# Optimization experiments

Measured on AMD Instinct MI355X. Metric: run time of the kernel, lower is better.

Reference implementation:

```python
import jax, jax.numpy as jnp
import numpy as np

D = 512  # link/path state dim == GRU hidden
R = 256  # readout dim
T = 8    # message-passing steps


def gru_cell(x, h, W_ih, W_hh, b_ih, b_hh):
    # torch nn.GRU cell math (weights stored [3H, in])
    gi = x @ W_ih.T + b_ih
    gh = h @ W_hh.T + b_hh
    i_r, i_z, i_n = jnp.split(gi, 3, axis=-1)
    h_r, h_z, h_n = jnp.split(gh, 3, axis=-1)
    r = jax.nn.sigmoid(i_r + h_r)
    z = jax.nn.sigmoid(i_z + h_z)
    n = jnp.tanh(i_n + r * h_n)
    return (1.0 - z) * n + z * h


def setup_inputs():
    key = jax.random.key(0)
    n_links, n_paths, L = 2000, 20000, 6
    ks = jax.random.split(key, 24)
    links = jax.random.randint(ks[0], (n_paths * L,), 0, n_links)
    paths = jnp.repeat(jnp.arange(n_paths), L)   # path id per entry
    seqs = jnp.tile(jnp.arange(L), n_paths)      # position of link within path
    link_capacity = jax.random.uniform(ks[1], (n_links, 1))
    bandwidth = jax.random.uniform(ks[2], (n_paths, 1))

    def u(k, shape, fan_in):
        s = 1.0 / np.sqrt(fan_in)
        return jax.random.uniform(k, shape, minval=-s, maxval=s)

    inp = dict(links=links, paths=paths, seqs=seqs,
               link_capacity=link_capacity, bandwidth=bandwidth)
    # path GRU (p_U) and link GRU (l_U)
    inp['Wih_p'] = u(ks[3], (3 * D, D), D); inp['Whh_p'] = u(ks[4], (3 * D, D), D)
    inp['bih_p'] = u(ks[5], (3 * D,), D);   inp['bhh_p'] = u(ks[6], (3 * D,), D)
    inp['Wih_l'] = u(ks[7], (3 * D, D), D); inp['Whh_l'] = u(ks[8], (3 * D, D), D)
    inp['bih_l'] = u(ks[9], (3 * D,), D);   inp['bhh_l'] = u(ks[10], (3 * D,), D)
    # readout MLPs (delay + jitter), torch Linear layout [out, in]
    inp['d_w1'] = u(ks[11], (R, D), D);      inp['d_b1'] = u(ks[12], (R,), D)
    inp['d_w2'] = u(ks[13], (R // 2, R), R); inp['d_b2'] = u(ks[14], (R // 2,), R)
    inp['d_w3'] = u(ks[15], (1, R // 2), R // 2); inp['d_b3'] = u(ks[16], (1,), R // 2)
    inp['j_w1'] = u(ks[17], (R, D), D);      inp['j_b1'] = u(ks[18], (R,), D)
    inp['j_w2'] = u(ks[19], (R // 2, R), R); inp['j_b2'] = u(ks[20], (R // 2,), R)
    inp['j_w3'] = u(ks[21], (1, R // 2), R // 2); inp['j_b3'] = u(ks[22], (1,), R // 2)
    inp['n_links'] = n_links
    inp['n_paths'] = n_paths
    inp['max_seq_len'] = L  # == max(seqs)+1
    return inp


def mlp(x, w1, b1, w2, b2, w3, b3):
    h = jax.nn.relu(x @ w1.T + b1)
    h = jax.nn.relu(h @ w2.T + b2)
    return h @ w3.T + b3


def reference(links, paths, seqs, link_capacity, bandwidth,
              Wih_p, Whh_p, bih_p, bhh_p, Wih_l, Whh_l, bih_l, bhh_l,
              d_w1, d_b1, d_w2, d_b2, d_w3, d_b3,
              j_w1, j_b1, j_w2, j_b2, j_w3, j_b3,
              n_links, n_paths, max_seq_len):
    dt = bandwidth.dtype
    path_h = jnp.concatenate([bandwidth, jnp.zeros((n_paths, D - 1), dt)], axis=1)
    link_h = jnp.concatenate([link_capacity, jnp.zeros((n_links, D - 1), dt)], axis=1)

    def p_step(h, x_t):
        h2 = gru_cell(x_t, h, Wih_p, Whh_p, bih_p, bhh_p)
        return h2, h2

    for _ in range(T):
        h_lp = link_h[links]  # gather link states onto path entries [E, D]
        x_seq = jnp.zeros((n_paths, max_seq_len, D), dt).at[paths, seqs].set(h_lp)
        path_h, outs = jax.lax.scan(p_step, path_h, jnp.swapaxes(x_seq, 0, 1))
        outs = jnp.swapaxes(outs, 0, 1)  # [n_paths, L, D] per-step path states
        msg = outs[paths, seqs]          # [E, D] message from each path position
        agg = jax.ops.segment_sum(msg, links, num_segments=n_links)  # scatter-add
        link_h = gru_cell(agg, link_h, Wih_l, Whh_l, bih_l, bhh_l)

    d = mlp(path_h, d_w1, d_b1, d_w2, d_b2, d_w3, d_b3)
    j = mlp(path_h, j_w1, j_b1, j_w2, j_b2, j_w3, j_b3)
    return d, j
```

## Files before the change

kernel.cpp:

```cpp
#include <hip/hip_runtime.h>
#include <stdint.h>

typedef __attribute__((ext_vector_type(4))) float float4v;
typedef __attribute__((ext_vector_type(2))) float float2v;
typedef __attribute__((ext_vector_type(8))) short short8v;

static __device__ __forceinline__ float sigp(float x){ return 1.f/(1.f+expf(-x)); }

static __device__ __forceinline__ unsigned short f2bf(float x){
  unsigned u = __float_as_uint(x);
  u += 0x7FFFu + ((u>>16)&1u);
  return (unsigned short)(u>>16);
}
static __device__ __forceinline__ float bf2f(unsigned short h){
  return __uint_as_float(((unsigned)h)<<16);
}

static __device__ __forceinline__ void gload16(const void* g, void* l){
  __builtin_amdgcn_global_load_lds((const __attribute__((address_space(1))) void*)g,
                                   (__attribute__((address_space(3))) void*)l, 16, 0, 0);
}

__global__ void sentf_k(float* __restrict__ o, int n, float v){
  int i = blockIdx.x*256 + threadIdx.x; if (i < n) o[i] = v;
}

__global__ void prep_k(const int* __restrict__ links, const int* __restrict__ paths,
                       const int* __restrict__ seqs, int* __restrict__ plink,
                       int* __restrict__ cnt){
  int e = blockIdx.x*256 + threadIdx.x;
  if (e < 120000){
    int p = paths[e], s = seqs[e], l = links[e];
    plink[p*6 + s] = l;
    atomicAdd(&cnt[s*2000 + l], 1);
  }
}
__global__ void scan_k(const int* __restrict__ cnt, int* __restrict__ off, int* __restrict__ cur){
  __shared__ int part[256]; __shared__ int pref[256];
  int t = threadIdx.x;
  int lo = t*47, hi = lo+47; if (hi > 12000) hi = 12000;
  int s = 0;
  for (int i=lo;i<hi;i++) s += cnt[i];
  part[t] = s; __syncthreads();
  if (t==0){ int r=0; for (int i=0;i<256;i++){ pref[i]=r; r+=part[i]; } }
  __syncthreads();
  int r = pref[t];
  for (int i=lo;i<hi;i++){ off[i]=r; cur[i]=r; r+=cnt[i]; }
}
__global__ void fill2_k(const int* __restrict__ links, const int* __restrict__ paths,
                        const int* __restrict__ seqs, int* __restrict__ cur,
                        int* __restrict__ plist){
  int e = blockIdx.x*256 + threadIdx.x;
  if (e < 120000){
    int p = paths[e], s = seqs[e], l = links[e];
    int pos = atomicAdd(&cur[s*2000 + l], 1);
    plist[pos] = p;
  }
}

__global__ void wcvt_k(const float* __restrict__ W, unsigned short* __restrict__ hi,
                       unsigned short* __restrict__ lo, int n){
  int i = blockIdx.x*256 + threadIdx.x;
  if (i < n){
    float x = W[i];
    unsigned short h = f2bf(x);
    hi[i] = h;
    lo[i] = f2bf(x - bf2f(h));
  }
}

__global__ void initp_k(const float* __restrict__ x0,
                        unsigned short* __restrict__ h0, unsigned short* __restrict__ l0,
                        unsigned short* __restrict__ h1, unsigned short* __restrict__ l1,
                        int Mreal){
  int i = blockIdx.x*256 + threadIdx.x;
  int m = i >> 9, c = i & 511;
  float v = (c==0 && m < Mreal) ? x0[m] : 0.f;
  unsigned short hh = f2bf(v);
  unsigned short ll = f2bf(v - bf2f(hh));
  h0[i]=hh; l0[i]=ll; h1[i]=hh; l1[i]=ll;
}

__global__ __launch_bounds__(512,4) void gmfma_k(
    const unsigned short* __restrict__ Ahi, const unsigned short* __restrict__ Alo,
    const unsigned short* __restrict__ Whi, const unsigned short* __restrict__ Wlo,
    const float* __restrict__ bias, const float* __restrict__ GI,
    const int* __restrict__ plink, int s,
    float* __restrict__ OutF,
    unsigned short* __restrict__ Ohi, unsigned short* __restrict__ Olo,
    int M, int gru, int writeF)
{
  __shared__ unsigned short sAh0[128*32], sAl0[128*32];
  __shared__ unsigned short sBh0[192*32], sBl0[192*32];
  __shared__ unsigned short sAh1[128*32], sAl1[128*32];
  __shared__ unsigned short sBh1[192*32], sBl1[192*32];
  const int tid  = threadIdx.x;
  const int lane = tid & 63, wave = tid >> 6;
  const int wm = wave >> 2, wn = wave & 3;
  const int bid = blockIdx.x;
  const int X = bid & 7, kk2 = bid >> 3;
  const int m0 = ((kk2 >> 3)*8 + X) * 128;
  const int cb = kk2 & 7;
  const int c16 = lane & 15, kq = lane >> 4;

  int offA;
  {
    int row = tid >> 2; int kg = (tid & 3) ^ ((row >> 1) & 3);
    offA = (m0 + row)*1024 + kg*16;
  }
  int offB0, offB1;
  {
    int gb = tid;
    int v  = gb >> 2;
    int kg = (gb & 3) ^ ((v >> 1) & 3);
    int wn_ = v / 48; int rem = v - wn_*48;
    int gg = rem >> 4, cc = rem & 15;
    offB0 = (gg*512 + cb*64 + wn_*16 + cc)*1024 + kg*16;
    gb = 512 + tid;
    v  = gb >> 2;
    kg = (gb & 3) ^ ((v >> 1) & 3);
    int wn2 = v / 48; rem = v - wn2*48;
    gg = rem >> 4; cc = rem & 15;
    if (wn2 > 3) wn2 = 3;
    offB1 = (gg*512 + cb*64 + wn2*16 + cc)*1024 + kg*16;
  }
  const int gA  = (wave*64)*8;
  const int gB0 = (wave*64)*8, gB1 = (512 + wave*64)*8;

  const int rA = wm*64 + c16;
  const int rdA = (rA*4 + (kq ^ ((rA>>1)&3)))*8;
  const int vB = wn*48 + c16;
  const int rdB = (vB*4 + (kq ^ ((vB>>1)&3)))*8;

  float4v acc[4][3];
#pragma unroll
  for (int i = 0; i < 4; ++i)
#pragma unroll
    for (int j = 0; j < 3; ++j) acc[i][j] = (float4v){0.f,0.f,0.f,0.f};

  auto STAGE = [&](int kb, unsigned short* dAh, unsigned short* dAl,
                   unsigned short* dBh, unsigned short* dBl){
    const int kbb = kb*64;
    const char* ah = (const char*)Ahi + kbb;
    const char* al = (const char*)Alo + kbb;
    const char* wh = (const char*)Whi + kbb;
    const char* wl = (const char*)Wlo + kbb;
    gload16(ah + offA, dAh + gA);
    gload16(al + offA, dAl + gA);
    gload16(wh + offB0, dBh + gB0);
    gload16(wl + offB0, dBl + gB0);
    if (tid < 256){
      gload16(wh + offB1, dBh + gB1);
      gload16(wl + offB1, dBl + gB1);
    }
  };

  auto COMPUTE = [&](const unsigned short* tAh, const unsigned short* tAl,
                     const unsigned short* tBh, const unsigned short* tBl){
    short8v ah[4], al[4], bh[3], bl[3];
#pragma unroll
    for (int mf = 0; mf < 4; ++mf) ah[mf] = *(const short8v*)(tAh + rdA + mf*512);
#pragma unroll
    for (int g = 0; g < 3; ++g)  bh[g]  = *(const short8v*)(tBh + rdB + g*512);
#pragma unroll
    for (int mf = 0; mf < 4; ++mf) al[mf] = *(const short8v*)(tAl + rdA + mf*512);
#pragma unroll
    for (int mf = 0; mf < 4; ++mf)
#pragma unroll
      for (int g = 0; g < 3; ++g)
        acc[mf][g] = __builtin_amdgcn_mfma_f32_16x16x32_bf16(ah[mf], bh[g], acc[mf][g], 0, 0, 0);
#pragma unroll
    for (int g = 0; g < 3; ++g)  bl[g]  = *(const short8v*)(tBl + rdB + g*512);
#pragma unroll
    for (int mf = 0; mf < 4; ++mf)
#pragma unroll
      for (int g = 0; g < 3; ++g)
        acc[mf][g] = __builtin_amdgcn_mfma_f32_16x16x32_bf16(al[mf], bh[g], acc[mf][g], 0, 0, 0);
#pragma unroll
    for (int mf = 0; mf < 4; ++mf)
#pragma unroll
      for (int g = 0; g < 3; ++g)
        acc[mf][g] = __builtin_amdgcn_mfma_f32_16x16x32_bf16(ah[mf], bl[g], acc[mf][g], 0, 0, 0);
  };

  STAGE(0, sAh0, sAl0, sBh0, sBl0);
  __syncthreads();
  for (int q = 0; q < 8; ++q){
    STAGE(2*q+1, sAh1, sAl1, sBh1, sBl1);
    COMPUTE(sAh0, sAl0, sBh0, sBl0);
    __syncthreads();
    if (q < 7) STAGE(2*q+2, sAh0, sAl0, sBh0, sBl0);
    COMPUTE(sAh1, sAl1, sBh1, sBl1);
    __syncthreads();
  }

  const int col = cb*64 + wn*16 + c16;
  if (!gru){
    const float b0f = bias[col], b1f = bias[512+col], b2f = bias[1024+col];
#pragma unroll
    for (int mf = 0; mf < 4; ++mf){
      const int mb = m0 + wm*64 + mf*16 + kq*4;
#pragma unroll
      for (int r = 0; r < 4; ++r){
        const int m = mb + r;
        if (m < M){
          float* c = OutF + (size_t)m*1536 + col;
          c[0]    = acc[mf][0][r] + b0f;
          c[512]  = acc[mf][1][r] + b1f;
          c[1024] = acc[mf][2][r] + b2f;
        }
      }
    }
  } else {
    const float br = bias[col], bz = bias[512+col], bn = bias[1024+col];
#pragma unroll
    for (int mf = 0; mf < 4; ++mf){
      const int mb = m0 + wm*64 + mf*16 + kq*4;
#pragma unroll
      for (int r = 0; r < 4; ++r){
        const int m = mb + r;
        if (m < M){
          const int gr = plink ? plink[m*6 + s] : m;
          const float* gi = GI + (size_t)gr*1536 + col;
          const size_t ix = (size_t)m*512 + col;
          float hold = bf2f(Ahi[ix]) + bf2f(Alo[ix]);
          float rr = sigp(gi[0]    + acc[mf][0][r] + br);
          float zz = sigp(gi[512]  + acc[mf][1][r] + bz);
          float nn = 2.f*sigp(2.f*(gi[1024] + rr*(acc[mf][2][r] + bn))) - 1.f;
          float h  = (1.f - zz)*nn + zz*hold;
          unsigned short hh = f2bf(h);
          Ohi[ix] = hh;
          Olo[ix] = f2bf(h - bf2f(hh));
          if (writeF) OutF[ix] = h;
        }
      }
    }
  }
}

__global__ __launch_bounds__(256,3) void rgemm_k(
    const unsigned short* __restrict__ Ahi, const unsigned short* __restrict__ Alo,
    const unsigned short* __restrict__ Whi, const unsigned short* __restrict__ Wlo,
    const float* __restrict__ bias,
    float* __restrict__ OutF,
    unsigned short* __restrict__ Ohi, unsigned short* __restrict__ Olo,
    int M, int N, int K, int relu)
{
  __shared__ unsigned short rAh0[128*32], rAl0[128*32], rWh0[64*32], rWl0[64*32];
  __shared__ unsigned short rAh1[128*32], rAl1[128*32], rWh1[64*32], rWl1[64*32];
  const int tid = threadIdx.x;
  const int lane = tid & 63, wave = tid >> 6;
  const int wm = wave >> 1, wn = wave & 1;
  const int m0 = blockIdx.x * 128, n0 = blockIdx.y * 64;
  const int c16 = lane & 15, kq = lane >> 4;
  const int K2 = K*2;

  int offA0, offA1, offW;
  { int g = tid;      int row = g>>2; int kg=(g&3)^((row>>1)&3); offA0 = (m0+row)*K2 + kg*16; }
  { int g = tid+256;  int row = g>>2; int kg=(g&3)^((row>>1)&3); offA1 = (m0+row)*K2 + kg*16; }
  { int g = tid;      int v = g>>2;   int kg=(g&3)^((v>>1)&3);   offW  = (n0+v)*K2 + kg*16; }
  const int gA0 = (wave*64)*8, gA1 = (wave*64+256)*8;
  const int gW  = (wave*64)*8;

  const int rA = wm*64 + c16;
  const int rdA = (rA*4 + (kq ^ ((rA>>1)&3)))*8;
  const int vB = wn*32 + c16;
  const int rdB = (vB*4 + (kq ^ ((vB>>1)&3)))*8;

  float4v acc[4][2];
#pragma unroll
  for (int i = 0; i < 4; ++i)
#pragma unroll
    for (int j = 0; j < 2; ++j) acc[i][j] = (float4v){0.f,0.f,0.f,0.f};

  auto STAGE = [&](int kb, unsigned short* dAh, unsigned short* dAl,
                   unsigned short* dWh, unsigned short* dWl){
    const int kbb = kb*64;
    gload16((const char*)Ahi + kbb + offA0, dAh + gA0);
    gload16((const char*)Ahi + kbb + offA1, dAh + gA1);
    gload16((const char*)Alo + kbb + offA0, dAl + gA0);
    gload16((const char*)Alo + kbb + offA1, dAl + gA1);
    gload16((const char*)Whi + kbb + offW, dWh + gW);
    gload16((const char*)Wlo + kbb + offW, dWl + gW);
  };

  auto COMPUTE = [&](const unsigned short* tAh, const unsigned short* tAl,
                     const unsigned short* tWh, const unsigned short* tWl){
    short8v ah[4], al[4], bh[2], bl[2];
#pragma unroll
    for (int mf = 0; mf < 4; ++mf) ah[mf] = *(const short8v*)(tAh + rdA + mf*512);
#pragma unroll
    for (int nf = 0; nf < 2; ++nf) bh[nf] = *(const short8v*)(tWh + rdB + nf*512);
#pragma unroll
    for (int mf = 0; mf < 4; ++mf) al[mf] = *(const short8v*)(tAl + rdA + mf*512);
#pragma unroll
    for (int mf = 0; mf < 4; ++mf)
#pragma unroll
      for (int nf = 0; nf < 2; ++nf)
        acc[mf][nf] = __builtin_amdgcn_mfma_f32_16x16x32_bf16(ah[mf], bh[nf], acc[mf][nf], 0, 0, 0);
#pragma unroll
    for (int nf = 0; nf < 2; ++nf) bl[nf] = *(const short8v*)(tWl + rdB + nf*512);
#pragma unroll
    for (int mf = 0; mf < 4; ++mf)
#pragma unroll
      for (int nf = 0; nf < 2; ++nf)
        acc[mf][nf] = __builtin_amdgcn_mfma_f32_16x16x32_bf16(al[mf], bh[nf], acc[mf][nf], 0, 0, 0);
#pragma unroll
    for (int mf = 0; mf < 4; ++mf)
#pragma unroll
      for (int nf = 0; nf < 2; ++nf)
        acc[mf][nf] = __builtin_amdgcn_mfma_f32_16x16x32_bf16(ah[mf], bl[nf], acc[mf][nf], 0, 0, 0);
  };

  const int nc = K >> 5;
  STAGE(0, rAh0, rAl0, rWh0, rWl0);
  __syncthreads();
  for (int q = 0; q < (nc>>1); ++q){
    STAGE(2*q+1, rAh1, rAl1, rWh1, rWl1);
    COMPUTE(rAh0, rAl0, rWh0, rWl0);
    __syncthreads();
    if (q < (nc>>1)-1) STAGE(2*q+2, rAh0, rAl0, rWh0, rWl0);
    COMPUTE(rAh1, rAl1, rWh1, rWl1);
    __syncthreads();
  }

#pragma unroll
  for (int nf = 0; nf < 2; ++nf){
    const int col = n0 + wn*32 + nf*16 + c16;
    const float b = bias[col];
#pragma unroll
    for (int mf = 0; mf < 4; ++mf){
      const int mb = m0 + wm*64 + mf*16 + kq*4;
#pragma unroll
      for (int r = 0; r < 4; ++r){
        const int m = mb + r;
        if (m < M){
          float v = acc[mf][nf][r] + b;
          if (relu) v = fmaxf(v, 0.f);
          const size_t ix = (size_t)m*N + col;
          if (OutF) OutF[ix] = v;
          if (Ohi){
            unsigned short hh = f2bf(v);
            Ohi[ix] = hh;
            Olo[ix] = f2bf(v - bf2f(hh));
          }
        }
      }
    }
  }
}

__global__ void aggv_k(const unsigned short* __restrict__ Hh, const unsigned short* __restrict__ Hl,
                       const int* __restrict__ plist,
                       const int* __restrict__ off, const int* __restrict__ cnt, int s,
                       float* __restrict__ AGG, int isFirst,
                       unsigned short* __restrict__ Ghi, unsigned short* __restrict__ Glo,
                       int emit)
{
  int l = blockIdx.x, t = threadIdx.x;
  size_t base = (size_t)l*512 + 2*t;
  if (l >= 2000){
    AGG[base] = 0.f; AGG[base+1] = 0.f;
    if (emit){ *(unsigned*)&Ghi[base] = 0u; *(unsigned*)&Glo[base] = 0u; }
    return;
  }
  int o = off[s*2000 + l], c = cnt[s*2000 + l];
  float a0 = isFirst ? 0.f : AGG[base];
  float a1 = isFirst ? 0.f : AGG[base+1];
  for (int i = 0; i < c; ++i){
    size_t p = (size_t)plist[o + i] * 512 + 2*t;
    unsigned hh = *(const unsigned*)(Hh + p);
    unsigned hl = *(const unsigned*)(Hl + p);
    a0 += __uint_as_float(hh << 16) + __uint_as_float(hl << 16);
    a1 += __uint_as_float(hh & 0xffff0000u) + __uint_as_float(hl & 0xffff0000u);
  }
  AGG[base] = a0; AGG[base+1] = a1;
  if (emit){
    unsigned short h0 = f2bf(a0), h1 = f2bf(a1);
    *(unsigned*)&Ghi[base] = (unsigned)h0 | ((unsigned)h1 << 16);
    unsigned short l0 = f2bf(a0 - bf2f(h0)), l1 = f2bf(a1 - bf2f(h1));
    *(unsigned*)&Glo[base] = (unsigned)l0 | ((unsigned)l1 << 16);
  }
}

__global__ void dotf_k(const float* __restrict__ T2, const float* __restrict__ w3,
                       const float* __restrict__ b3, float* __restrict__ out, int M)
{
  int lane = threadIdx.x & 63, w = threadIdx.x >> 6;
  int m = blockIdx.x * 4 + w;
  if (m >= M) return;
  float s = T2[(size_t)m*128 + lane] * w3[lane]
          + T2[(size_t)m*128 + 64 + lane] * w3[64 + lane];
#pragma unroll
  for (int off = 32; off; off >>= 1) s += __shfl_xor(s, off);
  if (lane == 0) out[m] = s + b3[0];
}

extern "C" void kernel_launch(void* const* d_in, const int* in_sizes, int n_in,
                              void* d_out, int out_size, void* d_ws, size_t ws_size,
                              hipStream_t stream)
{
  const int*   links = (const int*)d_in[0];
  const int*   paths = (const int*)d_in[1];
  const int*   seqs  = (const int*)d_in[2];
  const float* cap   = (const float*)d_in[3];
  const float* bw    = (const float*)d_in[4];
  const float* Wih_p = (const float*)d_in[5];
  const float* Whh_p = (const float*)d_in[6];
  const float* bih_p = (const float*)d_in[7];
  const float* bhh_p = (const float*)d_in[8];
  const float* Wih_l = (const float*)d_in[9];
  const float* Whh_l = (const float*)d_in[10];
  const float* bih_l = (const float*)d_in[11];
  const float* bhh_l = (const float*)d_in[12];
  const float* d_w1 = (const float*)d_in[13]; const float* d_b1 = (const float*)d_in[14];
  const float* d_w2 = (const float*)d_in[15]; const float* d_b2 = (const float*)d_in[16];
  const float* d_w3 = (const float*)d_in[17]; const float* d_b3 = (const float*)d_in[18];
  const float* j_w1 = (const float*)d_in[19]; const float* j_b1 = (const float*)d_in[20];
  const float* j_w2 = (const float*)d_in[21]; const float* j_b2 = (const float*)d_in[22];
  const float* j_w3 = (const float*)d_in[23]; const float* j_b3 = (const float*)d_in[24];
  float* out = (float*)d_out;

  const int MpP = 20480;
  const int MpL = 2048;
  char* p = (char*)d_ws;
  auto alloc = [&](size_t n){ char* r = p; p += (n + 255) & ~(size_t)255; return r; };
  unsigned short* Phi[2]; unsigned short* Plo[2];
  Phi[0] = (unsigned short*)alloc((size_t)MpP*512*2);
  Plo[0] = (unsigned short*)alloc((size_t)MpP*512*2);
  Phi[1] = (unsigned short*)alloc((size_t)MpP*512*2);
  Plo[1] = (unsigned short*)alloc((size_t)MpP*512*2);
  unsigned short* Lhi[2]; unsigned short* Llo[2];
  Lhi[0] = (unsigned short*)alloc((size_t)MpL*512*2);
  Llo[0] = (unsigned short*)alloc((size_t)MpL*512*2);
  Lhi[1] = (unsigned short*)alloc((size_t)MpL*512*2);
  Llo[1] = (unsigned short*)alloc((size_t)MpL*512*2);
  float* LG  = (float*)alloc((size_t)MpL*1536*4);
  float* AGG = (float*)alloc((size_t)MpL*512*4);
  unsigned short* AGh = (unsigned short*)alloc((size_t)MpL*512*2);
  unsigned short* AGl = (unsigned short*)alloc((size_t)MpL*512*2);
  unsigned short* WhhPh = (unsigned short*)alloc((size_t)1536*512*2);
  unsigned short* WhhPl = (unsigned short*)alloc((size_t)1536*512*2);
  unsigned short* WihPh = (unsigned short*)alloc((size_t)1536*512*2);
  unsigned short* WihPl = (unsigned short*)alloc((size_t)1536*512*2);
  unsigned short* WhhLh = (unsigned short*)alloc((size_t)1536*512*2);
  unsigned short* WhhLl = (unsigned short*)alloc((size_t)1536*512*2);
  unsigned short* WihLh = (unsigned short*)alloc((size_t)1536*512*2);
  unsigned short* WihLl = (unsigned short*)alloc((size_t)1536*512*2);
  unsigned short* DW1h = (unsigned short*)alloc((size_t)256*512*2);
  unsigned short* DW1l = (unsigned short*)alloc((size_t)256*512*2);
  unsigned short* DW2h = (unsigned short*)alloc((size_t)128*256*2);
  unsigned short* DW2l = (unsigned short*)alloc((size_t)128*256*2);
  unsigned short* JW1h = (unsigned short*)alloc((size_t)256*512*2);
  unsigned short* JW1l = (unsigned short*)alloc((size_t)256*512*2);
  unsigned short* JW2h = (unsigned short*)alloc((size_t)128*256*2);
  unsigned short* JW2l = (unsigned short*)alloc((size_t)128*256*2);
  int* cnt2  = (int*)alloc(12000*4);
  int* off2  = (int*)alloc(12000*4);
  int* cur2  = (int*)alloc(12000*4);
  int* plist = (int*)alloc(120000*4);
  int* plink = (int*)alloc(120000*4);
  unsigned short* t1h = Phi[1];
  unsigned short* t1l = Plo[1];
  float* t2 = LG;
  if ((size_t)(p - (char*)d_ws) > ws_size){
    sentf_k<<<(out_size+255)/256,256,0,stream>>>(out, out_size, 0.25f);
    return;
  }

  hipMemsetAsync(cnt2, 0, 12000*4, stream);
  prep_k<<<469,256,0,stream>>>(links, paths, seqs, plink, cnt2);
  scan_k<<<1,256,0,stream>>>(cnt2, off2, cur2);
  fill2_k<<<469,256,0,stream>>>(links, paths, seqs, cur2, plist);
  wcvt_k<<<3072,256,0,stream>>>(Whh_p, WhhPh, WhhPl, 1536*512);
  wcvt_k<<<3072,256,0,stream>>>(Wih_p, WihPh, WihPl, 1536*512);
  wcvt_k<<<3072,256,0,stream>>>(Whh_l, WhhLh, WhhLl, 1536*512);
  wcvt_k<<<3072,256,0,stream>>>(Wih_l, WihLh, WihLl, 1536*512);
  wcvt_k<<<512,256,0,stream>>>(d_w1, DW1h, DW1l, 256*512);
  wcvt_k<<<128,256,0,stream>>>(d_w2, DW2h, DW2l, 128*256);
  wcvt_k<<<512,256,0,stream>>>(j_w1, JW1h, JW1l, 256*512);
  wcvt_k<<<128,256,0,stream>>>(j_w2, JW2h, JW2l, 128*256);
  initp_k<<<(MpP*512)/256,256,0,stream>>>(bw,  Phi[0], Plo[0], Phi[1], Plo[1], 20000);
  initp_k<<<(MpL*512)/256,256,0,stream>>>(cap, Lhi[0], Llo[0], Lhi[1], Llo[1], 2000);

  int pb = 0, lb = 0;
  for (int t = 0; t < 8; ++t) {
    gmfma_k<<<16*8,512,0,stream>>>(Lhi[lb], Llo[lb], WihPh, WihPl, bih_p,
                                   (const float*)0, (const int*)0, 0,
                                   LG, (unsigned short*)0, (unsigned short*)0, 2000, 0, 0);
    for (int s6 = 0; s6 < 6; ++s6) {
      gmfma_k<<<160*8,512,0,stream>>>(Phi[pb], Plo[pb], WhhPh, WhhPl, bhh_p,
                                      LG, plink, s6,
                                      (float*)0, Phi[pb^1], Plo[pb^1], 20000, 1, 0);
      pb ^= 1;
      aggv_k<<<2048,256,0,stream>>>(Phi[pb], Plo[pb], plist, off2, cnt2, s6, AGG,
                                    (s6==0)?1:0, AGh, AGl, (s6==5)?1:0);
    }
    gmfma_k<<<16*8,512,0,stream>>>(AGh, AGl, WihLh, WihLl, bih_l,
                                   (const float*)0, (const int*)0, 0,
                                   LG, (unsigned short*)0, (unsigned short*)0, 2000, 0, 0);
    gmfma_k<<<16*8,512,0,stream>>>(Lhi[lb], Llo[lb], WhhLh, WhhLl, bhh_l,
                                   LG, (const int*)0, 0,
                                   (float*)0, Lhi[lb^1], Llo[lb^1], 2000, 1, 0);
    lb ^= 1;
  }

  rgemm_k<<<dim3(157,4),256,0,stream>>>(Phi[0], Plo[0], DW1h, DW1l, d_b1,
                                        (float*)0, t1h, t1l, 20000, 256, 512, 1);
  rgemm_k<<<dim3(157,2),256,0,stream>>>(t1h, t1l, DW2h, DW2l, d_b2,
                                        t2, (unsigned short*)0, (unsigned short*)0, 20000, 128, 256, 1);
  dotf_k<<<5000,256,0,stream>>>(t2, d_w3, d_b3, out, 20000);
  rgemm_k<<<dim3(157,4),256,0,stream>>>(Phi[0], Plo[0], JW1h, JW1l, j_b1,
                                        (float*)0, t1h, t1l, 20000, 256, 512, 1);
  rgemm_k<<<dim3(157,2),256,0,stream>>>(t1h, t1l, JW2h, JW2l, j_b2,
                                        t2, (unsigned short*)0, (unsigned short*)0, 20000, 128, 256, 1);
  dotf_k<<<5000,256,0,stream>>>(t2, j_w3, j_b3, out + 20000, 20000);
}
```

Baseline: 7.166 ms.

## Restructure split-bf16 GEMM as a single extended K loop over hi/lo passes

Instead of staging hi and lo copies of A and W together and issuing three MFMA products per K-block, the kernel now walks a K range three times as long (48 blocks): hi×hi, then lo×hi, then hi×lo. Each stage loads only one A and one B tile. This halves shared memory per block and cuts register pressure, and launch bounds are raised from 4 to 8 blocks per CU to gain occupancy. The trade-off is three times as many barriers and pipeline stages, with less MFMA work between syncs. The A activation tile is also reloaded from global memory on every pass.

Measured after the change: 20.13 ms. +180.9%, slower.

```diff
diff --git a/kernel.cpp b/kernel.cpp
--- a/kernel.cpp
+++ b/kernel.cpp
@@ -2,7 +2,6 @@
 #include <stdint.h>
 
 typedef __attribute__((ext_vector_type(4))) float float4v;
-typedef __attribute__((ext_vector_type(2))) float float2v;
 typedef __attribute__((ext_vector_type(8))) short short8v;
 
 static __device__ __forceinline__ float sigp(float x){ return 1.f/(1.f+expf(-x)); }
@@ -81,7 +80,7 @@
   h0[i]=hh; l0[i]=ll; h1[i]=hh; l1[i]=ll;
 }
 
-__global__ __launch_bounds__(512,4) void gmfma_k(
+__global__ __launch_bounds__(512,8) void gmfma_k(
     const unsigned short* __restrict__ Ahi, const unsigned short* __restrict__ Alo,
     const unsigned short* __restrict__ Whi, const unsigned short* __restrict__ Wlo,
     const float* __restrict__ bias, const float* __restrict__ GI,
@@ -90,10 +89,8 @@
     unsigned short* __restrict__ Ohi, unsigned short* __restrict__ Olo,
     int M, int gru, int writeF)
 {
-  __shared__ unsigned short sAh0[128*32], sAl0[128*32];
-  __shared__ unsigned short sBh0[192*32], sBl0[192*32];
-  __shared__ unsigned short sAh1[128*32], sAl1[128*32];
-  __shared__ unsigned short sBh1[192*32], sBl1[192*32];
+  __shared__ unsigned short sA0[128*32], sB0[192*32];
+  __shared__ unsigned short sA1[128*32], sB1[192*32];
   const int tid  = threadIdx.x;
   const int lane = tid & 63, wave = tid >> 6;
   const int wm = wave >> 2, wn = wave & 3;
@@ -138,59 +135,40 @@
 #pragma unroll
     for (int j = 0; j < 3; ++j) acc[i][j] = (float4v){0.f,0.f,0.f,0.f};
 
-  auto STAGE = [&](int kb, unsigned short* dAh, unsigned short* dAl,
-                   unsigned short* dBh, unsigned short* dBl){
-    const int kbb = kb*64;
-    const char* ah = (const char*)Ahi + kbb;
-    const char* al = (const char*)Alo + kbb;
-    const char* wh = (const char*)Whi + kbb;
-    const char* wl = (const char*)Wlo + kbb;
-    gload16(ah + offA, dAh + gA);
-    gload16(al + offA, dAl + gA);
-    gload16(wh + offB0, dBh + gB0);
-    gload16(wl + offB0, dBl + gB0);
+  auto STAGE = [&](int kb, unsigned short* dA, unsigned short* dB){
+    const unsigned short* As = (kb >= 16 && kb < 32) ? Alo : Ahi;
+    const unsigned short* Ws = (kb >= 32) ? Wlo : Whi;
+    const int kbb = (kb & 15)*64;
+    const char* ap = (const char*)As + kbb;
+    const char* wp = (const char*)Ws + kbb;
+    gload16(ap + offA, dA + gA);
+    gload16(wp + offB0, dB + gB0);
     if (tid < 256){
-      gload16(wh + offB1, dBh + gB1);
-      gload16(wl + offB1, dBl + gB1);
+      gload16(wp + offB1, dB + gB1);
     }
   };
 
-  auto COMPUTE = [&](const unsigned short* tAh, const unsigned short* tAl,
-                     const unsigned short* tBh, const unsigned short* tBl){
-    short8v ah[4], al[4], bh[3], bl[3];
-#pragma unroll
-    for (int mf = 0; mf < 4; ++mf) ah[mf] = *(const short8v*)(tAh + rdA + mf*512);
-#pragma unroll
-    for (int g = 0; g < 3; ++g)  bh[g]  = *(const short8v*)(tBh + rdB + g*512);
-#pragma unroll
-    for (int mf = 0; mf < 4; ++mf) al[mf] = *(const short8v*)(tAl + rdA + mf*512);
+  auto COMPUTE = [&](const unsigned short* tA, const unsigned short* tB){
+    short8v a[4], b[3];
+#pragma unroll
+    for (int mf = 0; mf < 4; ++mf) a[mf] = *(const short8v*)(tA + rdA + mf*512);
+#pragma unroll
+    for (int g = 0; g < 3; ++g)  b[g]  = *(const short8v*)(tB + rdB + g*512);
 #pragma unroll
     for (int mf = 0; mf < 4; ++mf)
 #pragma unroll
       for (int g = 0; g < 3; ++g)
-        acc[mf][g] = __builtin_amdgcn_mfma_f32_16x16x32_bf16(ah[mf], bh[g], acc[mf][g], 0, 0, 0);
-#pragma unroll
-    for (int g = 0; g < 3; ++g)  bl[g]  = *(const short8v*)(tBl + rdB + g*512);
-#pragma unroll
-    for (int mf = 0; mf < 4; ++mf)
-#pragma unroll
-      for (int g = 0; g < 3; ++g)
-        acc[mf][g] = __builtin_amdgcn_mfma_f32_16x16x32_bf16(al[mf], bh[g], acc[mf][g], 0, 0, 0);
-#pragma unroll
-    for (int mf = 0; mf < 4; ++mf)
-#pragma unroll
-      for (int g = 0; g < 3; ++g)
-        acc[mf][g] = __builtin_amdgcn_mfma_f32_16x16x32_bf16(ah[mf], bl[g], acc[mf][g], 0, 0, 0);
+        acc[mf][g] = __builtin_amdgcn_mfma_f32_16x16x32_bf16(a[mf], b[g], acc[mf][g], 0, 0, 0);
   };
 
-  STAGE(0, sAh0, sAl0, sBh0, sBl0);
+  STAGE(0, sA0, sB0);
   __syncthreads();
-  for (int q = 0; q < 8; ++q){
-    STAGE(2*q+1, sAh1, sAl1, sBh1, sBl1);
-    COMPUTE(sAh0, sAl0, sBh0, sBl0);
+  for (int q = 0; q < 24; ++q){
+    STAGE(2*q+1, sA1, sB1);
+    COMPUTE(sA0, sB0);
     __syncthreads();
-    if (q < 7) STAGE(2*q+2, sAh0, sAl0, sBh0, sBl0);
-    COMPUTE(sAh1, sAl1, sBh1, sBl1);
+    if (q < 23) STAGE(2*q+2, sA0, sB0);
+    COMPUTE(sA1, sB1);
     __syncthreads();
   }
 
```
